# Optimization experiments

Measured on AMD Instinct MI355X. Metric: run time of the kernel, lower is better.

## Reference

```python
import jax, jax.numpy as jnp
import numpy as np

B, C, H, W = 16, 256, 48, 160
BASELINE = 0.54
REL_ELEV = 1.65
H_MEAN = 1.535


def setup_inputs() -> dict:
    key = jax.random.key(0)
    k = jax.random.split(key, 5)
    features = jax.random.normal(k[0], (B, C, H, W), dtype=jnp.float32)
    # realistic KITTI-style P2 (full-resolution intrinsics; forward divides rows 0:2 by 16)
    base = np.zeros((3, 4), np.float32)
    base[0, 0] = 721.5; base[1, 1] = 721.5
    base[0, 2] = 609.5; base[1, 2] = 172.8
    base[2, 2] = 1.0;   base[1, 3] = 0.2
    P2 = jnp.asarray(base)[None] + 0.5 * jax.random.uniform(k[1], (B, 3, 4), dtype=jnp.float32)
    w_disp = 0.05 * jax.random.normal(k[2], (1, C, 3, 3), dtype=jnp.float32)  # disp_create conv3x3
    b_disp = jnp.zeros((1,), jnp.float32)
    w_ext = 0.05 * jax.random.normal(k[3], (C, C + 1), dtype=jnp.float32)     # extract conv1x1 (O,I)
    b_ext = jnp.zeros((C,), jnp.float32)
    alpha = 0.5 * jnp.ones((1,), jnp.float32)  # nn.Parameter (init 0.0; nonzero to exercise path)
    return {"features": features, "P2": P2, "w_disp": w_disp, "b_disp": b_disp,
            "w_ext": w_ext, "b_ext": b_ext, "alpha": alpha}


def _grid_sample_border(feat, gx, gy):
    """Bilinear grid_sample, padding_mode='border', align_corners=True.
    feat: (B,C1,H,W); gx, gy: (B,H,W) in [-1,1]."""
    Bs, C1, Hs, Ws = feat.shape
    ix = jnp.clip((gx + 1.0) * 0.5 * (Ws - 1), 0.0, Ws - 1)
    iy = jnp.clip((gy + 1.0) * 0.5 * (Hs - 1), 0.0, Hs - 1)
    ix0 = jnp.floor(ix); iy0 = jnp.floor(iy)
    ix1 = jnp.minimum(ix0 + 1.0, Ws - 1); iy1 = jnp.minimum(iy0 + 1.0, Hs - 1)
    wx = (ix - ix0).reshape(Bs, 1, -1)
    wy = (iy - iy0).reshape(Bs, 1, -1)
    flat = feat.reshape(Bs, C1, Hs * Ws)

    def gather(f, yq, xq):
        idx = (yq * Ws + xq).astype(jnp.int32).reshape(-1)
        return f[:, idx]  # (C1, H*W)

    g = jax.vmap(gather)
    v00 = g(flat, iy0, ix0); v01 = g(flat, iy0, ix1)
    v10 = g(flat, iy1, ix0); v11 = g(flat, iy1, ix1)
    out = (v00 * (1 - wx) * (1 - wy) + v01 * wx * (1 - wy)
           + v10 * (1 - wx) * wy + v11 * wx * wy)
    return out.reshape(Bs, C1, Hs, Ws)


def reference(features, P2, w_disp, b_disp, w_ext, b_ext, alpha):
    x = features
    Bs = x.shape[0]
    P2 = P2.at[:, 0:2].set(P2[:, 0:2] / 16.0)
    # disp_create: conv3x3 -> tanh, then detach-scaled
    d = jax.lax.conv_general_dilated(x, w_disp, (1, 1), 'SAME',
                                     dimension_numbers=('NCHW', 'OIHW', 'NCHW'))
    d = jnp.tanh(d + b_disp[None, :, None, None])
    disp = 0.1 * (0.05 * d + 0.95 * jax.lax.stop_gradient(d))  # (B,1,H,W)

    yy = jnp.arange(H, dtype=jnp.float32)[None, :, None]  # (1,H,1): row index
    fy = P2[:, 1:2, 1:2]; cy = P2[:, 1:2, 2:3]; Ty = P2[:, 1:2, 3:4]  # (B,1,1)
    disparity = jax.nn.relu(fy * BASELINE * (yy - cy)
                            / (jnp.abs(fy * REL_ELEV + Ty) + 1e-10))  # (B,H,1)
    disparity = jnp.broadcast_to(disparity, (Bs, H, W))

    x_base = jnp.broadcast_to(jnp.linspace(-1.0, 1.0, W, dtype=jnp.float32)[None, None, :], (Bs, H, W))
    y_base = jnp.linspace(-1.0, 1.0, H, dtype=jnp.float32)[None, :, None]  # (1,H,1)
    y_shifts_base = jax.nn.relu(H_MEAN * (yy - cy) / (2.0 * (REL_ELEV - 0.5 * H_MEAN))) / (H * 0.5)
    y_shifts = y_shifts_base + disp[:, 0]  # (B,H,W)
    gy = y_base + y_shifts

    feats = jnp.concatenate([disparity[:, None], x], axis=1)  # (B,C+1,H,W)
    samp = _grid_sample_border(feats, x_base, gy)
    out = jnp.einsum('oc,bchw->bohw', w_ext, samp) + b_ext[None, :, None, None]
    return jax.nn.relu(x + out * alpha[0])
```

## Files before the change

### kernel.cpp

```cpp
#include <hip/hip_runtime.h>
#include <stdint.h>

#define NB 16
#define NC 256
#define NH 48
#define NW 160
#define HW (NH*NW)
#define NP (NB*HW)

static __device__ __forceinline__ unsigned short f2bf(float f){
  union { float f; uint32_t u; } v; v.f = f;
  uint32_t u = v.u;
  uint32_t r = (u + 0x7FFFu + ((u >> 16) & 1u)) >> 16;
  return (unsigned short)r;
}
static __device__ __forceinline__ float bf2f(unsigned short h){
  union { float f; uint32_t u; } v; v.u = ((uint32_t)h) << 16; return v.f;
}

__global__ __launch_bounds__(256) void kw_conv(const float* __restrict__ w_ext,
                                               const float* __restrict__ w_disp,
                                               unsigned short* __restrict__ Wb,
                                               unsigned short* __restrict__ Wtap){
  if (blockIdx.x < 256){
    int idx = blockIdx.x * 256 + threadIdx.x;
    int o = idx >> 8, c = idx & 255;
    Wb[idx] = f2bf(w_ext[o * 257 + 1 + c]);
  } else {
    int c = threadIdx.x;
    #pragma unroll
    for (int m = 0; m < 16; ++m){
      float v = (m < 9) ? w_disp[c * 9 + m] : 0.f;
      Wtap[m * 256 + c] = f2bf(v);
    }
  }
}

typedef __attribute__((ext_vector_type(8))) short bf16x8;
typedef __attribute__((ext_vector_type(4))) float f32x4;

__global__ __launch_bounds__(256) void kb_gemm(
    const float* __restrict__ x,
    const unsigned short* __restrict__ Wb,
    const unsigned short* __restrict__ Wtap,
    unsigned short* __restrict__ U,
    float* __restrict__ T)
{
  __shared__ __align__(16) unsigned short smem[4 * 512];
  int bx = blockIdx.x;
  int b  = bx / 120;
  int nt = bx - b * 120;
  int p0 = nt * 64;

  int tid  = threadIdx.x;
  int lane = tid & 63;
  int w    = tid >> 6;
  int l15 = lane & 15;
  int lq  = lane >> 4;

  int sn  = tid & 63;
  int skq = tid >> 6;
  const float* xbase = x + ((size_t)b * NC) * HW + p0 + sn;
  unsigned short* swr = smem + (sn >> 4) * 512 + ((sn & 15) + skq * 16) * 8;

  f32x4 zero = {0.f, 0.f, 0.f, 0.f};
  f32x4 acc[4][4];
  f32x4 acct[4];
  #pragma unroll
  for (int mi = 0; mi < 4; ++mi){
    acct[mi] = zero;
    #pragma unroll
    for (int ni = 0; ni < 4; ++ni) acc[mi][ni] = zero;
  }

  for (int ks = 0; ks < 8; ++ks){
    __syncthreads();
    {
      int c0 = ks * 32 + skq * 8;
      const float* src = xbase + (size_t)c0 * HW;
      unsigned short h[8];
      #pragma unroll
      for (int j = 0; j < 8; ++j)
        h[j] = f2bf(src[(size_t)j * HW]);
      *(bf16x8*)swr = *(bf16x8*)h;
    }
    __syncthreads();

    bf16x8 af[4], bg[4];
    #pragma unroll
    for (int mi = 0; mi < 4; ++mi){
      int m = w * 64 + mi * 16 + l15;
      af[mi] = *(const bf16x8*)(Wb + (size_t)m * 256 + ks * 32 + lq * 8);
    }
    #pragma unroll
    for (int ni = 0; ni < 4; ++ni)
      bg[ni] = *(const bf16x8*)(smem + ni * 512 + lane * 8);

    #pragma unroll
    for (int mi = 0; mi < 4; ++mi)
      #pragma unroll
      for (int ni = 0; ni < 4; ++ni)
        acc[mi][ni] = __builtin_amdgcn_mfma_f32_16x16x32_bf16(af[mi], bg[ni], acc[mi][ni], 0, 0, 0);

    if (w == 0){
      bf16x8 at = *(const bf16x8*)(Wtap + (size_t)l15 * 256 + ks * 32 + lq * 8);
      #pragma unroll
      for (int ni = 0; ni < 4; ++ni)
        acct[ni] = __builtin_amdgcn_mfma_f32_16x16x32_bf16(at, bg[ni], acct[ni], 0, 0, 0);
    }
  }

  #pragma unroll
  for (int mi = 0; mi < 4; ++mi){
    #pragma unroll
    for (int ni = 0; ni < 4; ++ni){
      int o = w * 64 + mi * 16 + lq * 4;
      int n = ni * 16 + l15;
      size_t base = ((size_t)(b * NC + o)) * HW + p0 + n;
      #pragma unroll
      for (int r = 0; r < 4; ++r)
        U[base + (size_t)r * HW] = f2bf(acc[mi][ni][r]);
    }
  }
  if (w == 0){
    #pragma unroll
    for (int ni = 0; ni < 4; ++ni){
      int n = ni * 16 + l15;
      #pragma unroll
      for (int r = 0; r < 4; ++r){
        int k = lq * 4 + r;
        if (k < 9)
          T[(size_t)k * NP + (size_t)b * HW + p0 + n] = acct[ni][r];
      }
    }
  }
}

__global__ __launch_bounds__(256) void kp_grid(
    const float* __restrict__ P2, const float* __restrict__ b_disp,
    const float* __restrict__ T, float4* __restrict__ pre)
{
  int p = blockIdx.x * 256 + threadIdx.x;
  int b  = p / HW;
  int hw = p - b * HW;
  int y  = hw / NW;
  int xx = hw - y * NW;

  float d = 0.f;
  #pragma unroll
  for (int ky = 0; ky < 3; ++ky){
    int yy2 = y + ky - 1;
    if (yy2 < 0 || yy2 >= NH) continue;
    #pragma unroll
    for (int kx = 0; kx < 3; ++kx){
      int xx2 = xx + kx - 1;
      if (xx2 < 0 || xx2 >= NW) continue;
      d += T[(size_t)(ky * 3 + kx) * NP + b * HW + yy2 * NW + xx2];
    }
  }
  float th = tanhf(d + b_disp[0]);

  float fy = P2[b * 12 + 5] * 0.0625f;
  float cy = P2[b * 12 + 6] * 0.0625f;
  float Ty = P2[b * 12 + 7] * 0.0625f;

  float ysb   = fmaxf(1.535f * ((float)y - cy) / 1.765f, 0.f) * (1.f / 24.f);
  float ybase = -1.f + (float)y * (2.f / 47.f);
  float gy = ybase + ysb + 0.1f * th;
  float iy = fminf(fmaxf((gy + 1.f) * 0.5f * 47.f, 0.f), 47.f);
  float fiy0 = floorf(iy);
  float wy = iy - fiy0;
  int iy0 = (int)fiy0;
  int iy1 = min(iy0 + 1, 47);

  float inv_den = 1.f / (fabsf(fy * 1.65f + Ty) + 1e-10f);
  float dr0 = fmaxf(fy * 0.54f * ((float)iy0 - cy) * inv_den, 0.f);
  float dr1 = fmaxf(fy * 0.54f * ((float)iy1 - cy) * inv_den, 0.f);
  float dlerp = (1.f - wy) * dr0 + wy * dr1;

  float4 pr;
  pr.x = wy; pr.y = dlerp;
  pr.z = __int_as_float(iy0 * NW + xx);
  pr.w = __int_as_float(iy1 * NW + xx);
  pre[p] = pr;
}

__global__ __launch_bounds__(256) void kc_epilogue(
    const float* __restrict__ x, const float* __restrict__ w_ext,
    const float* __restrict__ b_ext, const float* __restrict__ alpha,
    const unsigned short* __restrict__ U, const float4* __restrict__ pre,
    float* __restrict__ out)
{
  int bx = blockIdx.x;
  int ptile = bx >> 3;
  int cg    = bx & 7;
  int p = ptile * 256 + threadIdx.x;
  int b  = p / HW;
  int hw = p - b * HW;

  float4 pr = pre[p];
  float wy    = pr.x;
  float dlerp = pr.y;
  int off0 = __float_as_int(pr.z);
  int off1 = __float_as_int(pr.w);
  float w1 = 1.f - wy;
  float al = alpha[0];

  size_t base0 = (size_t)(b * NC) * HW;
  const unsigned short* Ub = U + base0;
  const float* xb = x + base0 + hw;
  float* ob = out + base0 + hw;

  int o0 = cg * 32;
  #pragma unroll 4
  for (int o = o0; o < o0 + 32; ++o){
    float u0 = bf2f(Ub[(size_t)o * HW + off0]);
    float u1 = bf2f(Ub[(size_t)o * HW + off1]);
    float val = w1 * u0 + wy * u1 + w_ext[o * 257] * dlerp + b_ext[o];
    float r = xb[(size_t)o * HW] + al * val;
    ob[(size_t)o * HW] = fmaxf(r, 0.f);
  }
}

extern "C" void kernel_launch(void* const* d_in, const int* in_sizes, int n_in,
                              void* d_out, int out_size, void* d_ws, size_t ws_size,
                              hipStream_t stream) {
  const float* features = (const float*)d_in[0];
  const float* P2       = (const float*)d_in[1];
  const float* w_disp   = (const float*)d_in[2];
  const float* b_disp   = (const float*)d_in[3];
  const float* w_ext    = (const float*)d_in[4];
  const float* b_ext    = (const float*)d_in[5];
  const float* alpha    = (const float*)d_in[6];
  float* out = (float*)d_out;

  char* ws = (char*)d_ws;
  const size_t U_bytes   = (size_t)NP * 256 * 2;
  const size_t T_bytes   = (size_t)9 * NP * 4;
  const size_t pre_bytes = (size_t)NP * 16;
  unsigned short* U    = (unsigned short*)ws;
  float*          T    = (float*)(ws + U_bytes);
  float4*         pre  = (float4*)(ws + U_bytes + T_bytes);
  unsigned short* Wb   = (unsigned short*)(ws + U_bytes + T_bytes + pre_bytes);
  unsigned short* Wtap = Wb + 256 * 256;

  hipLaunchKernelGGL(kw_conv,     dim3(257),  dim3(256), 0, stream, w_ext, w_disp, Wb, Wtap);
  hipLaunchKernelGGL(kb_gemm,     dim3(1920), dim3(256), 0, stream, features, Wb, Wtap, U, T);
  hipLaunchKernelGGL(kp_grid,     dim3(480),  dim3(256), 0, stream, P2, b_disp, T, pre);
  hipLaunchKernelGGL(kc_epilogue, dim3(3840), dim3(256), 0, stream,
                     features, w_ext, b_ext, alpha, U, pre, out);
}
```

Before: 320.9 us.

## Double-buffer LDS and prefetch activations two K-steps ahead in GEMM

The GEMM kernel's K loop is fully unrolled and uses two LDS buffers. Register prefetch of the fp32 activation slices runs two iterations ahead, so global load latency overlaps with MFMA work. Each step now needs one barrier instead of two. The cost is more register pressure from two 8-float staging arrays, plus hand-placed waitcnt and sched barriers that constrain the compiler's scheduling.

```diff
diff --git a/kernel.cpp b/kernel.cpp
--- a/kernel.cpp
+++ b/kernel.cpp
@@ -46,7 +46,7 @@
     unsigned short* __restrict__ U,
     float* __restrict__ T)
 {
-  __shared__ __align__(16) unsigned short smem[4 * 512];
+  __shared__ __align__(16) unsigned short smem[2][4 * 512];
   int bx = blockIdx.x;
   int b  = bx / 120;
   int nt = bx - b * 120;
@@ -61,7 +61,7 @@
   int sn  = tid & 63;
   int skq = tid >> 6;
   const float* xbase = x + ((size_t)b * NC) * HW + p0 + sn;
-  unsigned short* swr = smem + (sn >> 4) * 512 + ((sn & 15) + skq * 16) * 8;
+  const int swroff = (sn >> 4) * 512 + ((sn & 15) + skq * 16) * 8;
 
   f32x4 zero = {0.f, 0.f, 0.f, 0.f};
   f32x4 acc[4][4];
@@ -73,42 +73,72 @@
     for (int ni = 0; ni < 4; ++ni) acc[mi][ni] = zero;
   }
 
-  for (int ks = 0; ks < 8; ++ks){
-    __syncthreads();
-    {
-      int c0 = ks * 32 + skq * 8;
-      const float* src = xbase + (size_t)c0 * HW;
-      unsigned short h[8];
-      #pragma unroll
-      for (int j = 0; j < 8; ++j)
-        h[j] = f2bf(src[(size_t)j * HW]);
-      *(bf16x8*)swr = *(bf16x8*)h;
-    }
-    __syncthreads();
-
-    bf16x8 af[4], bg[4];
-    #pragma unroll
-    for (int mi = 0; mi < 4; ++mi){
-      int m = w * 64 + mi * 16 + l15;
-      af[mi] = *(const bf16x8*)(Wb + (size_t)m * 256 + ks * 32 + lq * 8);
-    }
-    #pragma unroll
-    for (int ni = 0; ni < 4; ++ni)
-      bg[ni] = *(const bf16x8*)(smem + ni * 512 + lane * 8);
-
-    #pragma unroll
-    for (int mi = 0; mi < 4; ++mi)
-      #pragma unroll
-      for (int ni = 0; ni < 4; ++ni)
-        acc[mi][ni] = __builtin_amdgcn_mfma_f32_16x16x32_bf16(af[mi], bg[ni], acc[mi][ni], 0, 0, 0);
-
-    if (w == 0){
-      bf16x8 at = *(const bf16x8*)(Wtap + (size_t)l15 * 256 + ks * 32 + lq * 8);
-      #pragma unroll
-      for (int ni = 0; ni < 4; ++ni)
-        acct[ni] = __builtin_amdgcn_mfma_f32_16x16x32_bf16(at, bg[ni], acct[ni], 0, 0, 0);
-    }
-  }
+  float r0[8], r1[8];
+  #pragma unroll
+  for (int j = 0; j < 8; ++j) r0[j] = xbase[(size_t)(skq * 8 + j) * HW];
+  #pragma unroll
+  for (int j = 0; j < 8; ++j) r1[j] = xbase[(size_t)(32 + skq * 8 + j) * HW];
+  {
+    unsigned short h[8];
+    #pragma unroll
+    for (int j = 0; j < 8; ++j) h[j] = f2bf(r0[j]);
+    *(bf16x8*)(smem[0] + swroff) = *(bf16x8*)h;
+  }
+  asm volatile("s_waitcnt lgkmcnt(0)" ::: "memory");
+  __builtin_amdgcn_sched_barrier(0);
+  __builtin_amdgcn_s_barrier();
+  __builtin_amdgcn_sched_barrier(0);
+
+#define KB_ITER(T_, RCUR, RNXT)                                               \
+  {                                                                           \
+    constexpr int t_ = (T_);                                                  \
+    if (t_ + 2 < 8) {                                                         \
+      _Pragma("unroll")                                                       \
+      for (int j = 0; j < 8; ++j)                                             \
+        RCUR[j] = xbase[(size_t)((t_ + 2) * 32 + skq * 8 + j) * HW];          \
+    }                                                                         \
+    bf16x8 af[4], bg[4];                                                      \
+    _Pragma("unroll")                                                         \
+    for (int ni = 0; ni < 4; ++ni)                                            \
+      bg[ni] = *(const bf16x8*)(smem[t_ & 1] + ni * 512 + lane * 8);          \
+    _Pragma("unroll")                                                         \
+    for (int mi = 0; mi < 4; ++mi)                                            \
+      af[mi] = *(const bf16x8*)(Wb + (size_t)(w * 64 + mi * 16 + l15) * 256   \
+                                + t_ * 32 + lq * 8);                          \
+    _Pragma("unroll")                                                         \
+    for (int mi = 0; mi < 4; ++mi)                                            \
+      _Pragma("unroll")                                                       \
+      for (int ni = 0; ni < 4; ++ni)                                          \
+        acc[mi][ni] = __builtin_amdgcn_mfma_f32_16x16x32_bf16(af[mi], bg[ni], \
+                                                      acc[mi][ni], 0, 0, 0);  \
+    if (w == 0) {                                                             \
+      bf16x8 at = *(const bf16x8*)(Wtap + (size_t)l15 * 256 + t_ * 32 + lq * 8); \
+      _Pragma("unroll")                                                       \
+      for (int ni = 0; ni < 4; ++ni)                                          \
+        acct[ni] = __builtin_amdgcn_mfma_f32_16x16x32_bf16(at, bg[ni],        \
+                                                       acct[ni], 0, 0, 0);    \
+    }                                                                         \
+    if (t_ + 1 < 8) {                                                         \
+      unsigned short h[8];                                                    \
+      _Pragma("unroll")                                                       \
+      for (int j = 0; j < 8; ++j) h[j] = f2bf(RNXT[j]);                       \
+      *(bf16x8*)(smem[(t_ + 1) & 1] + swroff) = *(bf16x8*)h;                  \
+      asm volatile("s_waitcnt lgkmcnt(0)" ::: "memory");                      \
+      __builtin_amdgcn_sched_barrier(0);                                      \
+      __builtin_amdgcn_s_barrier();                                           \
+      __builtin_amdgcn_sched_barrier(0);                                      \
+    }                                                                         \
+  }
+
+  KB_ITER(0, r0, r1)
+  KB_ITER(1, r1, r0)
+  KB_ITER(2, r0, r1)
+  KB_ITER(3, r1, r0)
+  KB_ITER(4, r0, r1)
+  KB_ITER(5, r1, r0)
+  KB_ITER(6, r0, r1)
+  KB_ITER(7, r1, r0)
+#undef KB_ITER
 
   #pragma unroll
   for (int mi = 0; mi < 4; ++mi){
```

Measured after the change: 316.6 us. About the same (-1.4%).
